# Performance work log

Measured on AMD Instinct MI355X. Metric: run time of the kernel, lower is better.

The kernel has to match this reference:

```python
import jax, jax.numpy as jnp
import numpy as np

N_NODES = 50000
N_GRAPHS = 512


def _gcn_layer(x, src, dst, W, b):
    # DGL GraphConv, norm='both', allow_zero_in_degree=True
    n = x.shape[0]
    ones = jnp.ones(src.shape[0], x.dtype)
    deg_out = jnp.zeros(n, x.dtype).at[src].add(ones)
    deg_in = jnp.zeros(n, x.dtype).at[dst].add(ones)
    norm_out = jax.lax.rsqrt(jnp.maximum(deg_out, 1.0))
    norm_in = jax.lax.rsqrt(jnp.maximum(deg_in, 1.0))
    h = x * norm_out[:, None]
    agg = jax.ops.segment_sum(h[src], dst, num_segments=n)  # SpMM
    return (agg * norm_in[:, None]) @ W + b


def setup_inputs() -> dict:
    key = jax.random.key(0)
    ks = jax.random.split(key, 16)
    E = 800000
    inp = {
        'nid': jax.random.randint(ks[0], (N_NODES,), 0, 100000),
        'z': jax.random.randint(ks[1], (N_NODES,), 0, 1000),
        'src': jax.random.randint(ks[2], (E,), 0, N_NODES),
        'dst': jax.random.randint(ks[3], (E,), 0, N_NODES),
        'graph_id': jnp.sort(jax.random.randint(ks[4], (N_NODES,), 0, N_GRAPHS)),
        'init_embed': jax.random.normal(ks[5], (100000, 64), jnp.float32) * 0.1,
        'z_table': jax.random.normal(ks[6], (1000, 64), jnp.float32) * 0.1,
        'W0': jax.random.normal(ks[7], (128, 128), jnp.float32) * 0.1,
        'b0': jnp.zeros((128,), jnp.float32),
        'W1': jax.random.normal(ks[8], (128, 128), jnp.float32) * 0.1,
        'b1': jnp.zeros((128,), jnp.float32),
        'W2': jax.random.normal(ks[9], (128, 128), jnp.float32) * 0.1,
        'b2': jnp.zeros((128,), jnp.float32),
        'lin1_W': jax.random.normal(ks[10], (128, 128), jnp.float32) * 0.1,
        'lin1_b': jnp.zeros((128,), jnp.float32),
        'lin2_W': jax.random.normal(ks[11], (128, 200), jnp.float32) * 0.1,
        'lin2_b': jnp.zeros((200,), jnp.float32),
    }
    return inp


def reference(nid, z, src, dst, graph_id, init_embed, z_table, W0, b0, W1, b1, W2, b2, lin1_W, lin1_b, lin2_W, lin2_b):
    # node features: entity embedding lookup + structural label embedding, concat
    x = jnp.concatenate([init_embed[nid], z_table[z]], axis=1)  # [N, 128]
    # layers[:-1] with relu (dropout is identity in eval mode)
    x = jax.nn.relu(_gcn_layer(x, src, dst, W0, b0))
    x = jax.nn.relu(_gcn_layer(x, src, dst, W1, b1))
    x = _gcn_layer(x, src, dst, W2, b2)
    # SumPooling over subgraphs in the batch
    g = jax.ops.segment_sum(x, graph_id, num_segments=N_GRAPHS)  # [G, 128]
    h = jax.nn.relu(g @ lin1_W + lin1_b)
    return h @ lin2_W + lin2_b  # [G, num_rel]
```

## Files before the change

kernel.cpp:

```cpp
#include <hip/hip_runtime.h>
#include <hip/hip_bf16.h>


#define FEAT 128
#define NG 512
#define CH 128
#define NPMAX 12544
#define LDW 136

typedef __attribute__((ext_vector_type(8))) short bf16x8;
typedef __attribute__((ext_vector_type(4))) float f32x4;

__device__ __forceinline__ float bf2f(unsigned short u) {
    union { unsigned int i; float f; } v; v.i = ((unsigned int)u) << 16; return v.f;
}
__device__ __forceinline__ unsigned short f2bf(float f) {
    unsigned int u = __float_as_uint(f);
    return (unsigned short)((u + 0x7FFFu + ((u >> 16) & 1u)) >> 16);
}
__device__ __forceinline__ float lo16(unsigned u) { return __uint_as_float(u << 16); }
__device__ __forceinline__ float hi16(unsigned u) { return __uint_as_float(u & 0xFFFF0000u); }

__global__ __launch_bounds__(256) void k_hist(
        const int* __restrict__ src, const int* __restrict__ dst,
        unsigned* __restrict__ partial_out, unsigned* __restrict__ partial_in,
        int E, int NP, int Ec) {
    __shared__ unsigned h[NPMAX];
    int tid = threadIdx.x;
    int b = blockIdx.x;
    int c = b & (CH - 1);
    const int* __restrict__ arr = (b < CH) ? src : dst;
    unsigned* __restrict__ outp = ((b < CH) ? partial_out : partial_in) + (size_t)c * NP;
    for (int i = tid; i < NP; i += 256) h[i] = 0;
    __syncthreads();
    int e0 = c * Ec, e1 = min(E, e0 + Ec);
    for (int e = e0 + tid; e < e1; e += 256) {
        int v = arr[e];
        atomicAdd(&h[v >> 2], 1u << ((v & 3) * 8));
    }
    __syncthreads();
    for (int i = tid; i < NP; i += 256) outp[i] = h[i];
}

__global__ void k_merge(unsigned* __restrict__ partial_out, unsigned* __restrict__ partial_in,
                        int* __restrict__ cnt_in, float* __restrict__ norm_out,
                        float* __restrict__ norm_in, int N, int NP) {
    int w = blockIdx.x * blockDim.x + threadIdx.x;
    if (w >= NP) return;
    unsigned run_in = 0, run_out = 0;
    for (int c = 0; c < CH; c++) {
        size_t idx = (size_t)c * NP + w;
        unsigned v = partial_in[idx];
        partial_in[idx] = run_in;
        run_in += v;
        run_out += partial_out[idx];
    }
    #pragma unroll
    for (int j = 0; j < 4; j++) {
        int node = w * 4 + j;
        if (node < N) {
            unsigned di = (run_in  >> (j * 8)) & 255u;
            unsigned dd = (run_out >> (j * 8)) & 255u;
            cnt_in[node]   = (int)di;
            norm_in[node]  = rsqrtf(fmaxf((float)di, 1.0f));
            norm_out[node] = rsqrtf(fmaxf((float)dd, 1.0f));
        }
    }
}

__global__ void k_scan_local(const int* __restrict__ cnt, int* __restrict__ excl,
                             int* __restrict__ bsum, int N) {
    __shared__ int s[256];
    int x = threadIdx.x;
    int i = blockIdx.x * 256 + x;
    int v = (i < N) ? cnt[i] : 0;
    s[x] = v;
    __syncthreads();
    for (int off = 1; off < 256; off <<= 1) {
        int t = (x >= off) ? s[x - off] : 0;
        __syncthreads();
        s[x] += t;
        __syncthreads();
    }
    if (i < N) excl[i] = s[x] - v;
    if (x == 255) bsum[blockIdx.x] = s[255];
}

__global__ void k_scan_bsum_prep(int* __restrict__ bsum, int* __restrict__ boff, int nb,
                                 const float* __restrict__ W0, const float* __restrict__ W1,
                                 unsigned short* __restrict__ WF0, unsigned short* __restrict__ WF1) {
    if (blockIdx.x == 0) {
        __shared__ int s[256];
        int x = threadIdx.x;
        int v = (x < nb) ? bsum[x] : 0;
        s[x] = v;
        __syncthreads();
        for (int off = 1; off < 256; off <<= 1) {
            int t = (x >= off) ? s[x - off] : 0;
            __syncthreads();
            s[x] += t;
            __syncthreads();
        }
        if (x < nb) boff[x] = s[x] - v;
    } else {
        int t = ((int)blockIdx.x - 1) * 256 + threadIdx.x;
        const float* __restrict__ W = (t < 16384) ? W0 : W1;
        unsigned short* __restrict__ WF = (t < 16384) ? WF0 : WF1;
        int tt = t & 16383;
        int f = tt >> 9, l = (tt >> 3) & 63, e = tt & 7;
        int n = (f >> 2) * 16 + (l & 15);
        int k = (f & 3) * 32 + (l >> 4) * 8 + e;
        WF[tt] = f2bf(W[k * 128 + n]);
    }
}

__global__ void k_add_off(int* __restrict__ row_start, const int* __restrict__ boff,
                          float* __restrict__ g, int N) {
    int i = blockIdx.x * blockDim.x + threadIdx.x;
    int stride = gridDim.x * blockDim.x;
    if (i < N) row_start[i] += boff[i >> 8];
    for (int j = i; j < NG * FEAT; j += stride) g[j] = 0.f;
}

__global__ __launch_bounds__(256) void k_fill_bx(
        const int* __restrict__ src, const int* __restrict__ dst,
        const int* __restrict__ row_start, const unsigned* __restrict__ partial_in,
        unsigned short* __restrict__ csr,
        const int* __restrict__ nid, const int* __restrict__ z,
        const float* __restrict__ emb, const float* __restrict__ zt,
        const float* __restrict__ nout, unsigned short* __restrict__ x,
        int N, int E, int NP, int Ec) {
    if ((int)blockIdx.x < CH) {
        __shared__ unsigned cur[NPMAX];
        int tid = threadIdx.x;
        int c = blockIdx.x;
        const unsigned* __restrict__ pre = partial_in + (size_t)c * NP;
        for (int i = tid; i < NP; i += 256) cur[i] = pre[i];
        __syncthreads();
        int e0 = c * Ec, e1 = min(E, e0 + Ec);
        for (int e = e0 + tid; e < e1; e += 256) {
            int d = dst[e], s = src[e];
            int sh = (d & 3) * 8;
            unsigned t = atomicAdd(&cur[d >> 2], 1u << sh);
            int off = (int)((t >> sh) & 255u);
            csr[row_start[d] + off] = (unsigned short)s;
        }
    } else {
        int tid = ((int)blockIdx.x - CH) * 256 + threadIdx.x;
        int i = tid >> 5, q = tid & 31;
        if (i < N) {
            float4 v;
            if (q < 16) v = ((const float4*)emb)[(size_t)nid[i] * 16 + q];
            else        v = ((const float4*)zt)[(size_t)z[i] * 16 + (q - 16)];
            float w = nout[i];
            ushort4 u;
            u.x = f2bf(v.x * w); u.y = f2bf(v.y * w);
            u.z = f2bf(v.z * w); u.w = f2bf(v.w * w);
            ((ushort4*)x)[(size_t)i * 32 + q] = u;
        }
    }
}

#define ACC8(u)                                                                  \
    a0 += lo16(u.x); a1 += hi16(u.x); a2 += lo16(u.y); a3 += hi16(u.y);          \
    a4 += lo16(u.z); a5 += hi16(u.z); a6 += lo16(u.w); a7 += hi16(u.w);

#define GATHER_LOOP                                                              \
    {                                                                            \
        int base = row_start[node];                                              \
        int n = cnt_in[node];                                                    \
        const uint4* xp = (const uint4*)x;                   \
        for (int j0 = 0; j0 < n; j0 += 16) {                                     \
            int rem = n - j0;                                                    \
            int m = rem < 16 ? rem : 16;                                         \
            int e = (int)csr[base + j0 + (ql < m ? ql : 0)];                     \
            int j = 0;                                                           \
            for (; j + 8 <= m; j += 8) {                                         \
                int s0 = __shfl(e, j + 0, 16), s1 = __shfl(e, j + 1, 16);        \
                int s2 = __shfl(e, j + 2, 16), s3 = __shfl(e, j + 3, 16);        \
                int s4 = __shfl(e, j + 4, 16), s5 = __shfl(e, j + 5, 16);        \
                int s6 = __shfl(e, j + 6, 16), s7 = __shfl(e, j + 7, 16);        \
                uint4 u0 = xp[(size_t)s0 * 16 + ql];                             \
                uint4 u1 = xp[(size_t)s1 * 16 + ql];                             \
                uint4 u2 = xp[(size_t)s2 * 16 + ql];                             \
                uint4 u3 = xp[(size_t)s3 * 16 + ql];                             \
                uint4 u4 = xp[(size_t)s4 * 16 + ql];                             \
                uint4 u5 = xp[(size_t)s5 * 16 + ql];                             \
                uint4 u6 = xp[(size_t)s6 * 16 + ql];                             \
                uint4 u7 = xp[(size_t)s7 * 16 + ql];                             \
                ACC8(u0) ACC8(u1) ACC8(u2) ACC8(u3)                              \
                ACC8(u4) ACC8(u5) ACC8(u6) ACC8(u7)                              \
            }                                                                    \
            for (; j + 4 <= m; j += 4) {                                         \
                int s0 = __shfl(e, j + 0, 16), s1 = __shfl(e, j + 1, 16);        \
                int s2 = __shfl(e, j + 2, 16), s3 = __shfl(e, j + 3, 16);        \
                uint4 u0 = xp[(size_t)s0 * 16 + ql];                             \
                uint4 u1 = xp[(size_t)s1 * 16 + ql];                             \
                uint4 u2 = xp[(size_t)s2 * 16 + ql];                             \
                uint4 u3 = xp[(size_t)s3 * 16 + ql];                             \
                ACC8(u0) ACC8(u1) ACC8(u2) ACC8(u3)                              \
            }                                                                    \
            for (; j < m; j++) {                                                 \
                int s = __shfl(e, j, 16);                                        \
                uint4 u = xp[(size_t)s * 16 + ql];                               \
                ACC8(u)                                                          \
            }                                                                    \
        }                                                                        \
    }

__global__ __launch_bounds__(256) void k_gather_gemm(
        const unsigned short* __restrict__ x, const float* __restrict__ nin,
        const unsigned short* __restrict__ csr, const int* __restrict__ row_start,
        const int* __restrict__ cnt_in, const unsigned short* __restrict__ WF,
        const float* __restrict__ bias, const float* __restrict__ nout,
        unsigned short* __restrict__ y, int N) {
    __shared__ unsigned short As[64 * LDW];
    int tid = threadIdx.x;
    int nb = blockIdx.x * 64;
    int ql = tid & 15;
    int nsub = tid >> 4;

    #pragma unroll 1
    for (int r = 0; r < 4; r++) {
        int node = nb + r * 16 + nsub;
        float a0 = 0.f, a1 = 0.f, a2 = 0.f, a3 = 0.f;
        float a4 = 0.f, a5 = 0.f, a6 = 0.f, a7 = 0.f;
        if (node < N) {
            GATHER_LOOP
            float ni = nin[node];
            a0 *= ni; a1 *= ni; a2 *= ni; a3 *= ni;
            a4 *= ni; a5 *= ni; a6 *= ni; a7 *= ni;
        }
        uint4 o;
        o.x = (unsigned)f2bf(a0) | ((unsigned)f2bf(a1) << 16);
        o.y = (unsigned)f2bf(a2) | ((unsigned)f2bf(a3) << 16);
        o.z = (unsigned)f2bf(a4) | ((unsigned)f2bf(a5) << 16);
        o.w = (unsigned)f2bf(a6) | ((unsigned)f2bf(a7) << 16);
        *(uint4*)(As + (r * 16 + nsub) * LDW + ql * 8) = o;
    }
    __syncthreads();

    int lane = tid & 63;
    int m0 = (tid >> 6) * 16;
    int c = lane & 15, q = lane >> 4;

    const unsigned short* ap = As + (m0 + c) * LDW + q * 8;
    bf16x8 fa0 = *(const bf16x8*)(ap);
    bf16x8 fa1 = *(const bf16x8*)(ap + 32);
    bf16x8 fa2 = *(const bf16x8*)(ap + 64);
    bf16x8 fa3 = *(const bf16x8*)(ap + 96);
    const bf16x8* __restrict__ wf = (const bf16x8*)WF;

    #pragma unroll
    for (int nt = 0; nt < 8; nt++) {
        bf16x8 fb0 = wf[(nt * 4 + 0) * 64 + lane];
        bf16x8 fb1 = wf[(nt * 4 + 1) * 64 + lane];
        bf16x8 fb2 = wf[(nt * 4 + 2) * 64 + lane];
        bf16x8 fb3 = wf[(nt * 4 + 3) * 64 + lane];
        float bb = bias[nt * 16 + c];
        f32x4 acc = {bb, bb, bb, bb};
        acc = __builtin_amdgcn_mfma_f32_16x16x32_bf16(fa0, fb0, acc, 0, 0, 0);
        acc = __builtin_amdgcn_mfma_f32_16x16x32_bf16(fa1, fb1, acc, 0, 0, 0);
        acc = __builtin_amdgcn_mfma_f32_16x16x32_bf16(fa2, fb2, acc, 0, 0, 0);
        acc = __builtin_amdgcn_mfma_f32_16x16x32_bf16(fa3, fb3, acc, 0, 0, 0);
        #pragma unroll
        for (int rr = 0; rr < 4; rr++) {
            int row = m0 + q * 4 + rr;
            float s = nout[min(nb + row, N - 1)];
            As[row * LDW + nt * 16 + c] = f2bf(fmaxf(acc[rr], 0.f) * s);
        }
    }
    __syncthreads();

    for (int i = tid; i < 64 * 16; i += 256) {
        int row = i >> 4, seg = i & 15;
        int node = nb + row;
        if (node < N) {
            const ushort4* p = (const ushort4*)(As + row * LDW + seg * 8);
            ushort4* d = (ushort4*)(y + (size_t)node * 128 + seg * 8);
            d[0] = p[0]; d[1] = p[1];
        }
    }
}

__global__ __launch_bounds__(256) void k_gather_pool(
        const unsigned short* __restrict__ x, const float* __restrict__ nin,
        const unsigned short* __restrict__ csr, const int* __restrict__ row_start,
        const int* __restrict__ cnt_in, const int* __restrict__ gid,
        float* __restrict__ g, int N) {
    __shared__ float gl[16][FEAT];
    __shared__ int used;
    int tid = threadIdx.x;
    int nb = blockIdx.x * 16;
    for (int i = tid; i < 16 * FEAT; i += 256) ((float*)gl)[i] = 0.f;
    if (tid == 0) used = 0;
    __syncthreads();

    int ql = tid & 15;
    int node = nb + (tid >> 4);
    int g0 = gid[nb];
    float a0 = 0.f, a1 = 0.f, a2 = 0.f, a3 = 0.f;
    float a4 = 0.f, a5 = 0.f, a6 = 0.f, a7 = 0.f;
    int slot = -1;
    if (node < N) {
        GATHER_LOOP
        float ni = nin[node];
        a0 *= ni; a1 *= ni; a2 *= ni; a3 *= ni;
        a4 *= ni; a5 *= ni; a6 *= ni; a7 *= ni;
        slot = gid[node] - g0;
    }
    if (slot >= 16) {
        float* p = g + (size_t)(g0 + slot) * FEAT + ql * 8;
        atomicAdd(p + 0, a0); atomicAdd(p + 1, a1);
        atomicAdd(p + 2, a2); atomicAdd(p + 3, a3);
        atomicAdd(p + 4, a4); atomicAdd(p + 5, a5);
        atomicAdd(p + 6, a6); atomicAdd(p + 7, a7);
    } else if (slot >= 0) {
        float* p = &gl[slot][ql * 8];
        atomicAdd(p + 0, a0); atomicAdd(p + 1, a1);
        atomicAdd(p + 2, a2); atomicAdd(p + 3, a3);
        atomicAdd(p + 4, a4); atomicAdd(p + 5, a5);
        atomicAdd(p + 6, a6); atomicAdd(p + 7, a7);
        if (ql == 0) atomicOr(&used, 1 << slot);
    }
    __syncthreads();
    int u = used;
    #pragma unroll
    for (int s0 = 0; s0 < 16; s0 += 2) {
        int s = s0 + (tid >> 7);
        if ((u >> s) & 1) {
            int j = tid & 127;
            atomicAdd(&g[(size_t)(g0 + s) * FEAT + j], gl[s][j]);
        }
    }
}

__global__ __launch_bounds__(256) void k_head(
        const float* __restrict__ g, const int* __restrict__ gid,
        const float* __restrict__ W2, const float* __restrict__ b2,
        const float* __restrict__ l1W, const float* __restrict__ l1b,
        const float* __restrict__ l2W, const float* __restrict__ l2b,
        float* __restrict__ out, int N) {
    __shared__ float gs[128];
    __shared__ float ys[128];
    __shared__ float hs[128];
    int gi = blockIdx.x, tid = threadIdx.x;

    int lo = 0, hi = N;
    while (lo < hi) { int m = (lo + hi) >> 1; if (gid[m] < gi) lo = m + 1; else hi = m; }
    int s0 = lo;
    lo = 0; hi = N;
    while (lo < hi) { int m = (lo + hi) >> 1; if (gid[m] < gi + 1) lo = m + 1; else hi = m; }
    float cnt = (float)(lo - s0);

    if (tid < 128) gs[tid] = g[(size_t)gi * FEAT + tid];
    __syncthreads();
    if (tid < 128) {
        float a = cnt * b2[tid];
        for (int k = 0; k < 128; k++) a += gs[k] * W2[(size_t)k * 128 + tid];
        ys[tid] = a;
    }
    __syncthreads();
    if (tid < 128) {
        float a = l1b[tid];
        for (int k = 0; k < 128; k++) a += ys[k] * l1W[(size_t)k * 128 + tid];
        hs[tid] = fmaxf(a, 0.f);
    }
    __syncthreads();
    if (tid < 200) {
        float a = l2b[tid];
        for (int k = 0; k < 128; k++) a += hs[k] * l2W[(size_t)k * 200 + tid];
        out[(size_t)gi * 200 + tid] = a;
    }
}

extern "C" void kernel_launch(void* const* d_in, const int* in_sizes, int n_in,
                              void* d_out, int out_size, void* d_ws, size_t ws_size,
                              hipStream_t stream) {
    const int*   nid = (const int*)d_in[0];
    const int*   z   = (const int*)d_in[1];
    const int*   src = (const int*)d_in[2];
    const int*   dst = (const int*)d_in[3];
    const int*   gid = (const int*)d_in[4];
    const float* emb = (const float*)d_in[5];
    const float* zt  = (const float*)d_in[6];
    const float* W0  = (const float*)d_in[7];
    const float* b0  = (const float*)d_in[8];
    const float* W1  = (const float*)d_in[9];
    const float* b1  = (const float*)d_in[10];
    const float* W2  = (const float*)d_in[11];
    const float* b2  = (const float*)d_in[12];
    const float* l1W = (const float*)d_in[13];
    const float* l1b = (const float*)d_in[14];
    const float* l2W = (const float*)d_in[15];
    const float* l2b = (const float*)d_in[16];
    float* out = (float*)d_out;

    const int N = in_sizes[0];
    const int E = in_sizes[2];
    const int NB = (N + 255) / 256;
    const int NP = (N + 3) / 4;
    const int Ec = (E + CH - 1) / CH;

    size_t NA = (size_t)((N + 63) & ~63);
    float* norm_out = (float*)d_ws;
    float* norm_in  = norm_out + NA;
    float* g        = norm_in + NA;
    unsigned short* xA  = (unsigned short*)(g + (size_t)NG * FEAT);
    unsigned short* xB  = xA + (size_t)N * FEAT;
    unsigned short* WF0 = xB + (size_t)N * FEAT;
    unsigned short* WF1 = WF0 + 128 * 128;
    int* cnt_in    = (int*)(WF1 + 128 * 128);
    int* row_start = cnt_in + NA;
    int* bsum      = row_start + NA;
    int* boff      = bsum + 256;
    unsigned* partial_out = (unsigned*)(boff + 256);
    unsigned* partial_in  = partial_out + (size_t)CH * NP;
    unsigned short* csr = (unsigned short*)(partial_in + (size_t)CH * NP);

    k_hist<<<2 * CH, 256, 0, stream>>>(src, dst, partial_out, partial_in, E, NP, Ec);
    k_merge<<<(NP + 255) / 256, 256, 0, stream>>>(partial_out, partial_in, cnt_in,
                                                  norm_out, norm_in, N, NP);
    k_scan_local<<<NB, 256, 0, stream>>>(cnt_in, row_start, bsum, N);
    k_scan_bsum_prep<<<1 + 128, 256, 0, stream>>>(bsum, boff, NB, W0, W1, WF0, WF1);
    k_add_off<<<NB, 256, 0, stream>>>(row_start, boff, g, N);
    int XB = (N * 32 + 255) / 256;
    k_fill_bx<<<CH + XB, 256, 0, stream>>>(src, dst, row_start, partial_in, csr,
                                           nid, z, emb, zt, norm_out, xA, N, E, NP, Ec);

    int gg_blocks = (N + 63) / 64;
    int gp_blocks = (N + 15) / 16;

    k_gather_gemm<<<gg_blocks, 256, 0, stream>>>(xA, norm_in, csr, row_start, cnt_in,
                                                 WF0, b0, norm_out, xB, N);
    k_gather_gemm<<<gg_blocks, 256, 0, stream>>>(xB, norm_in, csr, row_start, cnt_in,
                                                 WF1, b1, norm_out, xA, N);
    k_gather_pool<<<gp_blocks, 256, 0, stream>>>(xA, norm_in, csr, row_start, cnt_in,
                                                 gid, g, N);

    k_head<<<NG, 256, 0, stream>>>(g, gid, W2, b2, l1W, l1b, l2W, l2b, out, N);
}
```

Before: 313.0 us.

## Unroll full 16-edge gather chunks, shrink CH, and rework pooling reduction

New measurement: 332.7 us. +6.3%, slower.

```diff
diff --git a/kernel.cpp b/kernel.cpp
--- a/kernel.cpp
+++ b/kernel.cpp
@@ -4,7 +4,7 @@
 
 #define FEAT 128
 #define NG 512
-#define CH 128
+#define CH 64
 #define NPMAX 12544
 #define LDW 136
 
@@ -170,12 +170,43 @@
         int base = row_start[node];                                              \
         int n = cnt_in[node];                                                    \
         const uint4* xp = (const uint4*)x;                   \
-        for (int j0 = 0; j0 < n; j0 += 16) {                                     \
-            int rem = n - j0;                                                    \
-            int m = rem < 16 ? rem : 16;                                         \
-            int e = (int)csr[base + j0 + (ql < m ? ql : 0)];                     \
+        int j0 = 0;                                                              \
+        for (; j0 + 16 <= n; j0 += 16) {                                         \
+            int e = (int)csr[base + j0 + ql];                                    \
+            int s0 = __shfl(e, 0, 16),   s1 = __shfl(e, 1, 16);                  \
+            int s2 = __shfl(e, 2, 16),   s3 = __shfl(e, 3, 16);                  \
+            int s4 = __shfl(e, 4, 16),   s5 = __shfl(e, 5, 16);                  \
+            int s6 = __shfl(e, 6, 16),   s7 = __shfl(e, 7, 16);                  \
+            int s8 = __shfl(e, 8, 16),   s9 = __shfl(e, 9, 16);                  \
+            int s10 = __shfl(e, 10, 16), s11 = __shfl(e, 11, 16);                \
+            int s12 = __shfl(e, 12, 16), s13 = __shfl(e, 13, 16);                \
+            int s14 = __shfl(e, 14, 16), s15 = __shfl(e, 15, 16);                \
+            uint4 u0  = xp[(size_t)s0 * 16 + ql];                                \
+            uint4 u1  = xp[(size_t)s1 * 16 + ql];                                \
+            uint4 u2  = xp[(size_t)s2 * 16 + ql];                                \
+            uint4 u3  = xp[(size_t)s3 * 16 + ql];                                \
+            uint4 u4  = xp[(size_t)s4 * 16 + ql];                                \
+            uint4 u5  = xp[(size_t)s5 * 16 + ql];                                \
+            uint4 u6  = xp[(size_t)s6 * 16 + ql];                                \
+            uint4 u7  = xp[(size_t)s7 * 16 + ql];                                \
+            uint4 u8  = xp[(size_t)s8 * 16 + ql];                                \
+            uint4 u9  = xp[(size_t)s9 * 16 + ql];                                \
+            uint4 u10 = xp[(size_t)s10 * 16 + ql];                               \
+            uint4 u11 = xp[(size_t)s11 * 16 + ql];                               \
+            uint4 u12 = xp[(size_t)s12 * 16 + ql];                               \
+            uint4 u13 = xp[(size_t)s13 * 16 + ql];                               \
+            uint4 u14 = xp[(size_t)s14 * 16 + ql];                               \
+            uint4 u15 = xp[(size_t)s15 * 16 + ql];                               \
+            ACC8(u0)  ACC8(u1)  ACC8(u2)  ACC8(u3)                               \
+            ACC8(u4)  ACC8(u5)  ACC8(u6)  ACC8(u7)                               \
+            ACC8(u8)  ACC8(u9)  ACC8(u10) ACC8(u11)                              \
+            ACC8(u12) ACC8(u13) ACC8(u14) ACC8(u15)                              \
+        }                                                                        \
+        int rem = n - j0;                                                        \
+        if (rem > 0) {                                                           \
+            int e = (int)csr[base + j0 + (ql < rem ? ql : 0)];                   \
             int j = 0;                                                           \
-            for (; j + 8 <= m; j += 8) {                                         \
+            for (; j + 8 <= rem; j += 8) {                                       \
                 int s0 = __shfl(e, j + 0, 16), s1 = __shfl(e, j + 1, 16);        \
                 int s2 = __shfl(e, j + 2, 16), s3 = __shfl(e, j + 3, 16);        \
                 int s4 = __shfl(e, j + 4, 16), s5 = __shfl(e, j + 5, 16);        \
@@ -191,7 +222,7 @@
                 ACC8(u0) ACC8(u1) ACC8(u2) ACC8(u3)                              \
                 ACC8(u4) ACC8(u5) ACC8(u6) ACC8(u7)                              \
             }                                                                    \
-            for (; j + 4 <= m; j += 4) {                                         \
+            for (; j + 4 <= rem; j += 4) {                                       \
                 int s0 = __shfl(e, j + 0, 16), s1 = __shfl(e, j + 1, 16);        \
                 int s2 = __shfl(e, j + 2, 16), s3 = __shfl(e, j + 3, 16);        \
                 uint4 u0 = xp[(size_t)s0 * 16 + ql];                             \
@@ -200,7 +231,7 @@
                 uint4 u3 = xp[(size_t)s3 * 16 + ql];                             \
                 ACC8(u0) ACC8(u1) ACC8(u2) ACC8(u3)                              \
             }                                                                    \
-            for (; j < m; j++) {                                                 \
+            for (; j < rem; j++) {                                               \
                 int s = __shfl(e, j, 16);                                        \
                 uint4 u = xp[(size_t)s * 16 + ql];                               \
                 ACC8(u)                                                          \
@@ -288,17 +319,14 @@
         const unsigned short* __restrict__ csr, const int* __restrict__ row_start,
         const int* __restrict__ cnt_in, const int* __restrict__ gid,
         float* __restrict__ g, int N) {
-    __shared__ float gl[16][FEAT];
-    __shared__ int used;
+    __shared__ __align__(16) float gl[16][132];
+    __shared__ int slots[16];
     int tid = threadIdx.x;
     int nb = blockIdx.x * 16;
-    for (int i = tid; i < 16 * FEAT; i += 256) ((float*)gl)[i] = 0.f;
-    if (tid == 0) used = 0;
-    __syncthreads();
-
     int ql = tid & 15;
-    int node = nb + (tid >> 4);
-    int g0 = gid[nb];
+    int nl = tid >> 4;
+    int node = nb + nl;
+
     float a0 = 0.f, a1 = 0.f, a2 = 0.f, a3 = 0.f;
     float a4 = 0.f, a5 = 0.f, a6 = 0.f, a7 = 0.f;
     int slot = -1;
@@ -307,32 +335,29 @@
         float ni = nin[node];
         a0 *= ni; a1 *= ni; a2 *= ni; a3 *= ni;
         a4 *= ni; a5 *= ni; a6 *= ni; a7 *= ni;
-        slot = gid[node] - g0;
-    }
-    if (slot >= 16) {
-        float* p = g + (size_t)(g0 + slot) * FEAT + ql * 8;
-        atomicAdd(p + 0, a0); atomicAdd(p + 1, a1);
-        atomicAdd(p + 2, a2); atomicAdd(p + 3, a3);
-        atomicAdd(p + 4, a4); atomicAdd(p + 5, a5);
-        atomicAdd(p + 6, a6); atomicAdd(p + 7, a7);
-    } else if (slot >= 0) {
-        float* p = &gl[slot][ql * 8];
-        atomicAdd(p + 0, a0); atomicAdd(p + 1, a1);
-        atomicAdd(p + 2, a2); atomicAdd(p + 3, a3);
-        atomicAdd(p + 4, a4); atomicAdd(p + 5, a5);
-        atomicAdd(p + 6, a6); atomicAdd(p + 7, a7);
-        if (ql == 0) atomicOr(&used, 1 << slot);
-    }
-    __syncthreads();
-    int u = used;
+        slot = gid[node];
+    }
+    float4* row = (float4*)&gl[nl][ql * 8];
+    row[0] = make_float4(a0, a1, a2, a3);
+    row[1] = make_float4(a4, a5, a6, a7);
+    if (ql == 0) slots[nl] = slot;
+    __syncthreads();
+
+    int h = tid >> 7;
+    int j = tid & 127;
+    int prev = -1;
+    float acc = 0.f;
     #pragma unroll
-    for (int s0 = 0; s0 < 16; s0 += 2) {
-        int s = s0 + (tid >> 7);
-        if ((u >> s) & 1) {
-            int j = tid & 127;
-            atomicAdd(&g[(size_t)(g0 + s) * FEAT + j], gl[s][j]);
-        }
-    }
+    for (int i = h * 8; i < h * 8 + 8; i++) {
+        int s = slots[i];
+        if (s != prev) {
+            if (prev >= 0) atomicAdd(&g[(size_t)prev * FEAT + j], acc);
+            acc = 0.f;
+            prev = s;
+        }
+        acc += gl[i][j];
+    }
+    if (prev >= 0) atomicAdd(&g[(size_t)prev * FEAT + j], acc);
 }
 
 __global__ __launch_bounds__(256) void k_head(
```
